# Kernel tuning notes

Measured on AMD Instinct MI355X. Metric: run time of the kernel, lower is better.

## Reference

```python
import jax, jax.numpy as jnp
import numpy as np

DIM = 512
HEAD_DIM = 32
HEADS = DIM // HEAD_DIM
WS = 7              # window_size
DISP = WS // 2      # cyclic shift displacement
SHIFTED = True


def _rel_indices(ws):
    # torch indexes pos_embedding with raw (possibly negative) distances;
    # negative python indices wrap modulo the dim size (2*ws-1).
    idx = np.array([[x, y] for x in range(ws) for y in range(ws)])
    d = idx[None, :, :] - idx[:, None, :]          # (ws^2, ws^2, 2)
    return np.mod(d, 2 * ws - 1)


def _mask(ws, disp, upper_lower, left_right):
    m = np.zeros((ws, ws, ws, ws), np.float32)
    if upper_lower:
        m[:-disp, :, -disp:, :] = -np.inf
        m[-disp:, :, :-disp, :] = -np.inf
    if left_right:
        m[:, -disp:, :, :-disp] = -np.inf
        m[:, :-disp, :, -disp:] = -np.inf
    return m.reshape(ws * ws, ws * ws)


def setup_inputs() -> dict:
    key = jax.random.key(0)
    ks = jax.random.split(key, 5)
    B, H, W = 32, 56, 56
    x = jax.random.normal(ks[0], (B, H, W, DIM), jnp.float32)
    w_qkv = jax.random.normal(ks[1], (DIM, 3 * DIM), jnp.float32) * 0.02
    pos_emb = jax.random.normal(ks[2], (2 * WS - 1, 2 * WS - 1, HEADS), jnp.float32)
    w_out = jax.random.normal(ks[3], (DIM, DIM), jnp.float32) * 0.02
    b_out = jax.random.normal(ks[4], (DIM,), jnp.float32) * 0.02
    return {"x": x, "w_qkv": w_qkv, "pos_emb": pos_emb, "w_out": w_out, "b_out": b_out}


def reference(x, w_qkv, pos_emb, w_out, b_out):
    rel = _rel_indices(WS)                         # static int constants
    ul_mask = jnp.asarray(_mask(WS, DISP, True, False))
    lr_mask = jnp.asarray(_mask(WS, DISP, False, True))

    B, H, W, _ = x.shape
    nw_h, nw_w = H // WS, W // WS

    if SHIFTED:
        x = jnp.roll(x, (-DISP, -DISP), axis=(1, 2))

    qkv = x @ w_qkv                                # (B,H,W,3*dim)

    def to_windows(t):
        # (B,H,W,dim) -> (B, heads, nw_h*nw_w, ws*ws, head_dim)
        t = t.reshape(B, nw_h, WS, nw_w, WS, HEADS, HEAD_DIM)
        return t.transpose(0, 5, 1, 3, 2, 4, 6).reshape(B, HEADS, nw_h * nw_w, WS * WS, HEAD_DIM)

    q, k, v = (to_windows(t) for t in jnp.split(qkv, 3, axis=-1))

    dots = jnp.einsum('bhwid,bhwjd->bhwij', q, k) * (HEAD_DIM ** -0.5)
    bias = pos_emb[rel[:, :, 0], rel[:, :, 1], :]  # (ws^2, ws^2, heads)
    dots = dots + bias.transpose(2, 0, 1)[None, :, None]

    if SHIFTED:
        dots = dots.at[:, :, -nw_w:].add(ul_mask)
        dots = dots.at[:, :, nw_w - 1::nw_w].add(lr_mask)

    attn = jax.nn.softmax(dots, axis=-1)
    out = jnp.einsum('bhwij,bhwjd->bhwid', attn, v)

    # (B,heads,nw,ws^2,d) -> (B,H,W,dim)
    out = out.reshape(B, HEADS, nw_h, nw_w, WS, WS, HEAD_DIM)
    out = out.transpose(0, 2, 4, 3, 5, 1, 6).reshape(B, H, W, DIM)
    out = out @ w_out + b_out

    if SHIFTED:
        out = jnp.roll(out, (DISP, DISP), axis=(1, 2))
    return out
```

## Files before the change

kernel.cpp:

```cpp
#include <hip/hip_runtime.h>
#include <hip/hip_bf16.h>
#include <stdint.h>


#define NWIN 64
#define NTOK 49
#define WIN_ELEMS 1568
#define HEAD_STRIDE 100352
#define BATCH_STRIDE 1605632
#define QKV_ELEMS 51380224
#define NTOKENS 100352
#define SCALE 0.17677669529663687f

typedef __attribute__((ext_vector_type(8))) short bf16x8;
typedef __attribute__((ext_vector_type(4))) float f32x4;

#define AS1 __attribute__((address_space(1)))
#define AS3 __attribute__((address_space(3)))

struct __align__(16) bf8 { __hip_bfloat16 h[8]; };

__device__ __forceinline__ void gload_lds16(const void* g, void* l) {
  __builtin_amdgcn_global_load_lds((const AS1 unsigned int*)g,
                                   (AS3 unsigned int*)l, 16, 0, 0);
}

__device__ __forceinline__ void token_decode(int t, int& b, int& i, int& j) {
  b = t / 3136;
  int r = t - b * 3136;
  i = r / 56;
  j = r - i * 56;
}

__global__ __launch_bounds__(256) void k_prep_lut(int* __restrict__ lutw,
                                                  int* __restrict__ luto) {
  int t = blockIdx.x * 256 + threadIdx.x;
  int b, i, j;
  token_decode(t, b, i, j);
  int win = (i / 7) * 8 + (j / 7);
  int pos = (i % 7) * 7 + (j % 7);
  lutw[t] = b * BATCH_STRIDE + win * WIN_ELEMS + pos * 32;
  int di = i + 3; if (di >= 56) di -= 56;
  int dj = j + 3; if (dj >= 56) dj -= 56;
  luto[t] = ((b * 56 + di) * 56 + dj) * 512;
}

__global__ __launch_bounds__(256) void k_prep_x(const float* __restrict__ x,
                                                __hip_bfloat16* __restrict__ xb) {
  int idx = blockIdx.x * 256 + threadIdx.x;
  int t = idx >> 6;
  int g = idx & 63;
  int b, i, j;
  token_decode(t, b, i, j);
  int si = i + 3; if (si >= 56) si -= 56;
  int sj = j + 3; if (sj >= 56) sj -= 56;
  const float* src = x + ((size_t)(b * 56 + si) * 56 + sj) * 512 + g * 8;
  float4 a0 = *(const float4*)src;
  float4 a1 = *(const float4*)(src + 4);
  bf8 o;
  o.h[0] = __float2bfloat16(a0.x); o.h[1] = __float2bfloat16(a0.y);
  o.h[2] = __float2bfloat16(a0.z); o.h[3] = __float2bfloat16(a0.w);
  o.h[4] = __float2bfloat16(a1.x); o.h[5] = __float2bfloat16(a1.y);
  o.h[6] = __float2bfloat16(a1.z); o.h[7] = __float2bfloat16(a1.w);
  int slot = ((g * 8) ^ ((t & 7) << 3));
  *(bf8*)(xb + (size_t)t * 512 + slot) = o;
}

__global__ __launch_bounds__(256) void k_transpose(const float* __restrict__ in,
                                                   __hip_bfloat16* __restrict__ out,
                                                   int K, int N) {
  __shared__ float tl[64][65];
  const int nb = blockIdx.x * 64, kb = blockIdx.y * 64;
  const int tid = threadIdx.x;
#pragma unroll
  for (int s = 0; s < 16; ++s) {
    int idx = s * 256 + tid; int r = idx >> 6, c = idx & 63;
    tl[r][c] = in[(size_t)(kb + r) * N + nb + c];
  }
  __syncthreads();
#pragma unroll
  for (int s = 0; s < 16; ++s) {
    int idx = s * 256 + tid; int r = idx >> 6, c = idx & 63;
    int row = nb + r;
    int col = (kb + c) ^ ((row & 7) << 3);
    out[(size_t)row * K + col] = __float2bfloat16(tl[c][r]);
  }
}

__global__ __launch_bounds__(256) void k_prep_bias(const float* __restrict__ pe,
                                                   float* __restrict__ biasT) {
  int id = blockIdx.x * 256 + threadIdx.x;
  int whid = id >> 12;
  int wtype = whid >> 4, h = whid & 15;
  int mid = id & 4095;
  int mf = mid >> 10, r = (mid >> 8) & 3, lane = (mid >> 2) & 63, nf = mid & 3;
  int key = mf * 16 + (lane >> 4) * 4 + r;
  int query = nf * 16 + (lane & 15);
  float v;
  if (key >= 49 || query >= 49) {
    v = -1e30f;
  } else {
    int i = query, j = key;
    int xi = i / 7, yi = i - xi * 7;
    int xj = j / 7, yj = j - xj * 7;
    int dx = xj - xi; if (dx < 0) dx += 13;
    int dy = yj - yi; if (dy < 0) dy += 13;
    v = pe[(dx * 13 + dy) * 16 + h];
    if ((wtype & 1) && ((xi >= 4) != (xj >= 4))) v = -1e30f;
    if ((wtype & 2) && ((yi >= 4) != (yj >= 4))) v = -1e30f;
  }
  biasT[id] = v;
}

__global__ __launch_bounds__(256) void k_qkv_mfma(
    const __hip_bfloat16* __restrict__ xb, const __hip_bfloat16* __restrict__ wbt,
    const int* __restrict__ lutw,
    __hip_bfloat16* __restrict__ qb, __hip_bfloat16* __restrict__ kb,
    __hip_bfloat16* __restrict__ vb) {
  __shared__ __align__(16) short As[2][128 * 64];
  __shared__ __align__(16) short Bs[2][128 * 64];
  const int tid = threadIdx.x;
  const int lid = blockIdx.x;
  const int wid = (lid & 7) * 1176 + (lid >> 3);
  const int t0 = (wid / 12) * 128;
  const int n0 = (wid % 12) * 128;
  const int lane = tid & 63, wave = tid >> 6;
  const int wm = wave >> 1, wn = wave & 1;

  const __hip_bfloat16* asrc[4];
  const __hip_bfloat16* bsrc[4];
#pragma unroll
  for (int s = 0; s < 4; ++s) {
    int c = s * 256 + tid;
    int row = c >> 3, kc = c & 7;
    asrc[s] = xb + (size_t)(t0 + row) * 512 + kc * 8;
    bsrc[s] = wbt + (size_t)(n0 + row) * 512 + kc * 8;
  }

  f32x4 acc[4][4] = {};
  const int arow = wm * 64 + (lane & 15);
  const int brow = wn * 64 + (lane & 15);
  const int koff = (lane >> 4) * 8;
  const int sw = (lane & 7) << 3;

#pragma unroll
  for (int s = 0; s < 4; ++s) {
    gload_lds16(asrc[s], (char*)As[0] + wave * 1024 + s * 4096);
    gload_lds16(bsrc[s], (char*)Bs[0] + wave * 1024 + s * 4096);
  }

  for (int t = 0; t < 8; ++t) {
    const int buf = t & 1;
    if (t < 7) {
      const int kt = (t + 1) * 64;
#pragma unroll
      for (int s = 0; s < 4; ++s) {
        gload_lds16(asrc[s] + kt, (char*)As[buf ^ 1] + wave * 1024 + s * 4096);
        gload_lds16(bsrc[s] + kt, (char*)Bs[buf ^ 1] + wave * 1024 + s * 4096);
      }
      asm volatile("s_waitcnt vmcnt(8)" ::: "memory");
    } else {
      asm volatile("s_waitcnt vmcnt(0)" ::: "memory");
    }
    __builtin_amdgcn_s_barrier();
    __builtin_amdgcn_sched_barrier(0);

    bf16x8 af[2][4], bfr[2][4];
#pragma unroll
    for (int kk = 0; kk < 2; ++kk) {
      const int eo = (kk * 32 + koff) ^ sw;
#pragma unroll
      for (int mf = 0; mf < 4; ++mf)
        af[kk][mf] = *(const bf16x8*)&As[buf][(arow + mf * 16) * 64 + eo];
#pragma unroll
      for (int nf = 0; nf < 4; ++nf)
        bfr[kk][nf] = *(const bf16x8*)&Bs[buf][(brow + nf * 16) * 64 + eo];
    }
    __builtin_amdgcn_s_setprio(1);
#pragma unroll
    for (int kk = 0; kk < 2; ++kk)
#pragma unroll
      for (int mf = 0; mf < 4; ++mf)
#pragma unroll
        for (int nf = 0; nf < 4; ++nf)
          acc[mf][nf] = __builtin_amdgcn_mfma_f32_16x16x32_bf16(
              af[kk][mf], bfr[kk][nf], acc[mf][nf], 0, 0, 0);
    __builtin_amdgcn_s_setprio(0);
    __builtin_amdgcn_s_barrier();
    __builtin_amdgcn_sched_barrier(0);
  }

  __hip_bfloat16* obs[4];
#pragma unroll
  for (int nf = 0; nf < 4; ++nf) {
    int n = n0 + wn * 64 + nf * 16 + (lane & 15);
    int sp = n >> 9, hc = n & 511, h = hc >> 5, d = hc & 31;
    obs[nf] = (sp == 0 ? qb : (sp == 1 ? kb : vb)) + (size_t)h * HEAD_STRIDE + d;
  }
  const int tbase = t0 + wm * 64 + (lane >> 4) * 4;
  int woff[4][4];
#pragma unroll
  for (int mf = 0; mf < 4; ++mf)
#pragma unroll
    for (int r = 0; r < 4; ++r)
      woff[mf][r] = lutw[tbase + mf * 16 + r];
#pragma unroll
  for (int mf = 0; mf < 4; ++mf)
#pragma unroll
    for (int r = 0; r < 4; ++r) {
      size_t off = (size_t)woff[mf][r];
#pragma unroll
      for (int nf = 0; nf < 4; ++nf)
        obs[nf][off] = __float2bfloat16(acc[mf][nf][r]);
    }
}

__global__ __launch_bounds__(256) void k_attn_mfma(
    const __hip_bfloat16* __restrict__ qb, const __hip_bfloat16* __restrict__ kb,
    const __hip_bfloat16* __restrict__ vb, const float* __restrict__ biasT,
    __hip_bfloat16* __restrict__ ab) {
  __shared__ __align__(16) __hip_bfloat16 P[4][64 * 72];
  __shared__ __align__(16) __hip_bfloat16 VT[4][32 * 64];
  const int tid = threadIdx.x, lane = tid & 63, wave = tid >> 6;
  const int gid = blockIdx.x * 4 + wave;
  const int win = gid & 63, h = (gid >> 6) & 15;
  const int wtype = (((win >> 3) == 7) ? 1 : 0) | (((win & 7) == 7) ? 2 : 0);
  const size_t qkbase = (size_t)gid * WIN_ELEMS;
  const int fr = lane & 15, fo = (lane >> 4) * 8;

  bf8 v8[4];
#pragma unroll
  for (int it = 0; it < 4; ++it) {
    int c = it * 64 + lane;
    if (c < 196) v8[it] = *(const bf8*)(vb + qkbase + (size_t)c * 8);
  }

  bf16x8 kf[4], qf[4];
#pragma unroll
  for (int f = 0; f < 4; ++f) {
    kf[f] = *(const bf16x8*)(kb + qkbase + (size_t)(f * 16 + fr) * 32 + fo);
    qf[f] = *(const bf16x8*)(qb + qkbase + (size_t)(f * 16 + fr) * 32 + fo);
  }

  __hip_bfloat16* vtw = VT[wave];
  {
    bf16x8 zz = {};
#pragma unroll
    for (int z = 0; z < 4; ++z) *(bf16x8*)&vtw[z * 512 + lane * 8] = zz;
  }
#pragma unroll
  for (int it = 0; it < 4; ++it) {
    int c = it * 64 + lane;
    if (c < 196) {
      int pos = c >> 2, d0 = (c & 3) * 8;
#pragma unroll
      for (int u = 0; u < 8; ++u) {
        int d = d0 + u;
        vtw[d * 64 + (pos ^ ((d & 7) << 3))] = v8[it].h[u];
      }
    }
  }

  f32x4 sacc[4][4] = {};
#pragma unroll
  for (int mf = 0; mf < 4; ++mf)
#pragma unroll
    for (int nf = 0; nf < 4; ++nf)
      sacc[mf][nf] = __builtin_amdgcn_mfma_f32_16x16x32_bf16(
          kf[mf], qf[nf], sacc[mf][nf], 0, 0, 0);

  const float* bp = biasT + (size_t)(wtype * 16 + h) * 4096;
#pragma unroll
  for (int mf = 0; mf < 4; ++mf)
#pragma unroll
    for (int r = 0; r < 4; ++r) {
      float4 bv = *(const float4*)(bp + ((mf * 4 + r) * 64 + lane) * 4);
      sacc[mf][0][r] = fmaf(sacc[mf][0][r], SCALE, bv.x);
      sacc[mf][1][r] = fmaf(sacc[mf][1][r], SCALE, bv.y);
      sacc[mf][2][r] = fmaf(sacc[mf][2][r], SCALE, bv.z);
      sacc[mf][3][r] = fmaf(sacc[mf][3][r], SCALE, bv.w);
    }

  float inv[4];
#pragma unroll
  for (int nf = 0; nf < 4; ++nf) {
    float m = sacc[0][nf][0];
#pragma unroll
    for (int mf = 0; mf < 4; ++mf)
#pragma unroll
      for (int r = 0; r < 4; ++r) m = fmaxf(m, sacc[mf][nf][r]);
    m = fmaxf(m, __shfl_xor(m, 16));
    m = fmaxf(m, __shfl_xor(m, 32));
    float sum = 0.f;
#pragma unroll
    for (int mf = 0; mf < 4; ++mf)
#pragma unroll
      for (int r = 0; r < 4; ++r) {
        float e = __expf(sacc[mf][nf][r] - m);
        sacc[mf][nf][r] = e;
        sum += e;
      }
    sum += __shfl_xor(sum, 16);
    sum += __shfl_xor(sum, 32);
    inv[nf] = 1.0f / sum;
  }

  __hip_bfloat16* pw = P[wave];
#pragma unroll
  for (int mf = 0; mf < 4; ++mf)
#pragma unroll
    for (int r = 0; r < 4; ++r) {
      int key = mf * 16 + (lane >> 4) * 4 + r;
#pragma unroll
      for (int nf = 0; nf < 4; ++nf) {
        int query = nf * 16 + fr;
        pw[query * 72 + key] = __float2bfloat16(sacc[mf][nf][r] * inv[nf]);
      }
    }

  f32x4 oacc[4][2] = {};
#pragma unroll
  for (int kk = 0; kk < 2; ++kk) {
    bf16x8 vf[2];
#pragma unroll
    for (int n2 = 0; n2 < 2; ++n2) {
      int d = n2 * 16 + fr;
      vf[n2] = *(const bf16x8*)&vtw[d * 64 + ((kk * 32 + fo) ^ ((d & 7) << 3))];
    }
#pragma unroll
    for (int mf = 0; mf < 4; ++mf) {
      bf16x8 pa = *(const bf16x8*)&pw[(mf * 16 + fr) * 72 + kk * 32 + fo];
#pragma unroll
      for (int n2 = 0; n2 < 2; ++n2)
        oacc[mf][n2] = __builtin_amdgcn_mfma_f32_16x16x32_bf16(
            pa, vf[n2], oacc[mf][n2], 0, 0, 0);
    }
  }

#pragma unroll
  for (int mf = 0; mf < 4; ++mf)
#pragma unroll
    for (int r = 0; r < 4; ++r) {
      int row = mf * 16 + (lane >> 4) * 4 + r;
      if (row < 49) {
#pragma unroll
        for (int n2 = 0; n2 < 2; ++n2)
          ab[qkbase + (size_t)row * 32 + n2 * 16 + fr] =
              __float2bfloat16(oacc[mf][n2][r]);
      }
    }
}

__global__ __launch_bounds__(256) void k_out_mfma(
    const __hip_bfloat16* __restrict__ ab, const __hip_bfloat16* __restrict__ wot,
    const int* __restrict__ lutw, const int* __restrict__ luto,
    const float* __restrict__ bias, float* __restrict__ out) {
  __shared__ __align__(16) short As[2][128 * 64];
  __shared__ __align__(16) short Bs[2][128 * 64];
  const int tid = threadIdx.x;
  const int lid = blockIdx.x;
  const int wid = (lid & 7) * 392 + (lid >> 3);
  const int t0 = (wid >> 2) * 128;
  const int n0 = (wid & 3) * 128;
  const int lane = tid & 63, wave = tid >> 6;
  const int wm = wave >> 1, wn = wave & 1;

  size_t aoff[4];
  const __hip_bfloat16* bsrc[4];
#pragma unroll
  for (int s = 0; s < 4; ++s) {
    int c = s * 256 + tid;
    int row = c >> 3, kc = c & 7;
    aoff[s] = (size_t)lutw[t0 + row] + (size_t)(kc >> 2) * HEAD_STRIDE + (kc & 3) * 8;
    bsrc[s] = wot + (size_t)(n0 + row) * 512 + kc * 8;
  }

  f32x4 acc[4][4] = {};
  const int arow = wm * 64 + (lane & 15);
  const int brow = wn * 64 + (lane & 15);
  const int koff = (lane >> 4) * 8;
  const int sw = (lane & 7) << 3;

#pragma unroll
  for (int s = 0; s < 4; ++s) {
    gload_lds16(ab + aoff[s], (char*)As[0] + wave * 1024 + s * 4096);
    gload_lds16(bsrc[s], (char*)Bs[0] + wave * 1024 + s * 4096);
  }

  for (int t = 0; t < 8; ++t) {
    const int buf = t & 1;
    if (t < 7) {
      const int kt = (t + 1) * 64;
      size_t hoff = (size_t)(kt >> 5) * HEAD_STRIDE;
#pragma unroll
      for (int s = 0; s < 4; ++s) {
        gload_lds16(ab + aoff[s] + hoff, (char*)As[buf ^ 1] + wave * 1024 + s * 4096);
        gload_lds16(bsrc[s] + kt, (char*)Bs[buf ^ 1] + wave * 1024 + s * 4096);
      }
      asm volatile("s_waitcnt vmcnt(8)" ::: "memory");
    } else {
      asm volatile("s_waitcnt vmcnt(0)" ::: "memory");
    }
    __builtin_amdgcn_s_barrier();
    __builtin_amdgcn_sched_barrier(0);

    bf16x8 af[2][4], bfr[2][4];
#pragma unroll
    for (int kk = 0; kk < 2; ++kk) {
      const int eo = kk * 32 + koff;
#pragma unroll
      for (int mf = 0; mf < 4; ++mf)
        af[kk][mf] = *(const bf16x8*)&As[buf][(arow + mf * 16) * 64 + eo];
#pragma unroll
      for (int nf = 0; nf < 4; ++nf)
        bfr[kk][nf] = *(const bf16x8*)&Bs[buf][(brow + nf * 16) * 64 + (eo ^ sw)];
    }
    __builtin_amdgcn_s_setprio(1);
#pragma unroll
    for (int kk = 0; kk < 2; ++kk)
#pragma unroll
      for (int mf = 0; mf < 4; ++mf)
#pragma unroll
        for (int nf = 0; nf < 4; ++nf)
          acc[mf][nf] = __builtin_amdgcn_mfma_f32_16x16x32_bf16(
              af[kk][mf], bfr[kk][nf], acc[mf][nf], 0, 0, 0);
    __builtin_amdgcn_s_setprio(0);
    __builtin_amdgcn_s_barrier();
    __builtin_amdgcn_sched_barrier(0);
  }

  float bia[4];
#pragma unroll
  for (int nf = 0; nf < 4; ++nf)
    bia[nf] = bias[n0 + wn * 64 + nf * 16 + (lane & 15)];

  const int tbase = t0 + wm * 64 + (lane >> 4) * 4;
  int ooff[4][4];
#pragma unroll
  for (int mf = 0; mf < 4; ++mf)
#pragma unroll
    for (int r = 0; r < 4; ++r)
      ooff[mf][r] = luto[tbase + mf * 16 + r];
#pragma unroll
  for (int mf = 0; mf < 4; ++mf) {
#pragma unroll
    for (int r = 0; r < 4; ++r) {
      float* op = out + (size_t)ooff[mf][r] + n0 + wn * 64 + (lane & 15);
#pragma unroll
      for (int nf = 0; nf < 4; ++nf) op[nf * 16] = acc[mf][nf][r] + bia[nf];
    }
  }
}

extern "C" void kernel_launch(void* const* d_in, const int* in_sizes, int n_in,
                              void* d_out, int out_size, void* d_ws, size_t ws_size,
                              hipStream_t stream) {
  const float* x     = (const float*)d_in[0];
  const float* w_qkv = (const float*)d_in[1];
  const float* pe    = (const float*)d_in[2];
  const float* w_out = (const float*)d_in[3];
  const float* b_out = (const float*)d_in[4];
  float* out = (float*)d_out;

  __hip_bfloat16* qb  = (__hip_bfloat16*)d_ws;
  __hip_bfloat16* kb  = qb + (size_t)QKV_ELEMS;
  __hip_bfloat16* vb  = kb + (size_t)QKV_ELEMS;
  __hip_bfloat16* xb  = vb + (size_t)QKV_ELEMS;
  __hip_bfloat16* ab  = xb;
  __hip_bfloat16* wbt = xb + (size_t)QKV_ELEMS;
  __hip_bfloat16* wot = wbt + (size_t)(1536 * 512);
  float* biasT = (float*)(wot + (size_t)(512 * 512));
  int* lutw = (int*)(biasT + 262144);
  int* luto = lutw + NTOKENS;

  k_prep_lut<<<dim3(392), dim3(256), 0, stream>>>(lutw, luto);
  k_prep_x<<<dim3(25088), dim3(256), 0, stream>>>(x, xb);
  k_transpose<<<dim3(24, 8), dim3(256), 0, stream>>>(w_qkv, wbt, 512, 1536);
  k_transpose<<<dim3(8, 8), dim3(256), 0, stream>>>(w_out, wot, 512, 512);
  k_prep_bias<<<dim3(1024), dim3(256), 0, stream>>>(pe, biasT);
  k_qkv_mfma<<<dim3(9408), dim3(256), 0, stream>>>(xb, wbt, lutw, qb, kb, vb);
  k_attn_mfma<<<dim3(8192), dim3(256), 0, stream>>>(qb, kb, vb, biasT, ab);
  k_out_mfma<<<dim3(3136), dim3(256), 0, stream>>>(ab, wot, lutw, luto, b_out, out);
}
```

Baseline: 542.4 us.

## Fuse shifted fp32-to-bf16 input conversion into QKV GEMM A-tile loading

```diff
diff --git a/kernel.cpp b/kernel.cpp
--- a/kernel.cpp
+++ b/kernel.cpp
@@ -32,38 +32,28 @@
   j = r - i * 56;
 }
 
-__global__ __launch_bounds__(256) void k_prep_lut(int* __restrict__ lutw,
+__device__ __forceinline__ bf8 pack8(const float4& a, const float4& b) {
+  bf8 o;
+  o.h[0] = __float2bfloat16(a.x); o.h[1] = __float2bfloat16(a.y);
+  o.h[2] = __float2bfloat16(a.z); o.h[3] = __float2bfloat16(a.w);
+  o.h[4] = __float2bfloat16(b.x); o.h[5] = __float2bfloat16(b.y);
+  o.h[6] = __float2bfloat16(b.z); o.h[7] = __float2bfloat16(b.w);
+  return o;
+}
+
+__global__ __launch_bounds__(256) void k_prep_lut(int* __restrict__ lutr,
+                                                  int* __restrict__ lutw,
                                                   int* __restrict__ luto) {
   int t = blockIdx.x * 256 + threadIdx.x;
   int b, i, j;
   token_decode(t, b, i, j);
+  int si = i + 3; if (si >= 56) si -= 56;
+  int sj = j + 3; if (sj >= 56) sj -= 56;
+  lutr[t] = ((b * 56 + si) * 56 + sj) * 512;
   int win = (i / 7) * 8 + (j / 7);
   int pos = (i % 7) * 7 + (j % 7);
   lutw[t] = b * BATCH_STRIDE + win * WIN_ELEMS + pos * 32;
-  int di = i + 3; if (di >= 56) di -= 56;
-  int dj = j + 3; if (dj >= 56) dj -= 56;
-  luto[t] = ((b * 56 + di) * 56 + dj) * 512;
-}
-
-__global__ __launch_bounds__(256) void k_prep_x(const float* __restrict__ x,
-                                                __hip_bfloat16* __restrict__ xb) {
-  int idx = blockIdx.x * 256 + threadIdx.x;
-  int t = idx >> 6;
-  int g = idx & 63;
-  int b, i, j;
-  token_decode(t, b, i, j);
-  int si = i + 3; if (si >= 56) si -= 56;
-  int sj = j + 3; if (sj >= 56) sj -= 56;
-  const float* src = x + ((size_t)(b * 56 + si) * 56 + sj) * 512 + g * 8;
-  float4 a0 = *(const float4*)src;
-  float4 a1 = *(const float4*)(src + 4);
-  bf8 o;
-  o.h[0] = __float2bfloat16(a0.x); o.h[1] = __float2bfloat16(a0.y);
-  o.h[2] = __float2bfloat16(a0.z); o.h[3] = __float2bfloat16(a0.w);
-  o.h[4] = __float2bfloat16(a1.x); o.h[5] = __float2bfloat16(a1.y);
-  o.h[6] = __float2bfloat16(a1.z); o.h[7] = __float2bfloat16(a1.w);
-  int slot = ((g * 8) ^ ((t & 7) << 3));
-  *(bf8*)(xb + (size_t)t * 512 + slot) = o;
+  luto[t] = lutr[t];
 }
 
 __global__ __launch_bounds__(256) void k_transpose(const float* __restrict__ in,
@@ -113,8 +103,8 @@
 }
 
 __global__ __launch_bounds__(256) void k_qkv_mfma(
-    const __hip_bfloat16* __restrict__ xb, const __hip_bfloat16* __restrict__ wbt,
-    const int* __restrict__ lutw,
+    const float* __restrict__ x, const __hip_bfloat16* __restrict__ wbt,
+    const int* __restrict__ lutr, const int* __restrict__ lutw,
     __hip_bfloat16* __restrict__ qb, __hip_bfloat16* __restrict__ kb,
     __hip_bfloat16* __restrict__ vb) {
   __shared__ __align__(16) short As[2][128 * 64];
@@ -127,13 +117,19 @@
   const int lane = tid & 63, wave = tid >> 6;
   const int wm = wave >> 1, wn = wave & 1;
 
-  const __hip_bfloat16* asrc[4];
+  const int arow_s = tid >> 1, half = tid & 1;
+  const float* axp = x + (size_t)lutr[t0 + arow_s] + half * 32;
+  short* aw[2] = { &As[0][arow_s * 64], &As[1][arow_s * 64] };
+  int wch[4];
+#pragma unroll
+  for (int c = 0; c < 4; ++c)
+    wch[c] = ((half * 4 + c) ^ (arow_s & 7)) * 8;
+
   const __hip_bfloat16* bsrc[4];
 #pragma unroll
   for (int s = 0; s < 4; ++s) {
     int c = s * 256 + tid;
     int row = c >> 3, kc = c & 7;
-    asrc[s] = xb + (size_t)(t0 + row) * 512 + kc * 8;
     bsrc[s] = wbt + (size_t)(n0 + row) * 512 + kc * 8;
   }
 
@@ -143,22 +139,28 @@
   const int koff = (lane >> 4) * 8;
   const int sw = (lane & 7) << 3;
 
-#pragma unroll
-  for (int s = 0; s < 4; ++s) {
-    gload_lds16(asrc[s], (char*)As[0] + wave * 1024 + s * 4096);
+  float4 ar[8];
+#pragma unroll
+  for (int u = 0; u < 8; ++u) ar[u] = ((const float4*)axp)[u];
+#pragma unroll
+  for (int s = 0; s < 4; ++s)
     gload_lds16(bsrc[s], (char*)Bs[0] + wave * 1024 + s * 4096);
-  }
+#pragma unroll
+  for (int c = 0; c < 4; ++c)
+    *(bf8*)(aw[0] + wch[c]) = pack8(ar[2 * c], ar[2 * c + 1]);
+  asm volatile("s_waitcnt lgkmcnt(0)" ::: "memory");
 
   for (int t = 0; t < 8; ++t) {
     const int buf = t & 1;
     if (t < 7) {
       const int kt = (t + 1) * 64;
-#pragma unroll
-      for (int s = 0; s < 4; ++s) {
-        gload_lds16(asrc[s] + kt, (char*)As[buf ^ 1] + wave * 1024 + s * 4096);
+      const float* p = axp + kt;
+#pragma unroll
+      for (int u = 0; u < 8; ++u) ar[u] = ((const float4*)p)[u];
+#pragma unroll
+      for (int s = 0; s < 4; ++s)
         gload_lds16(bsrc[s] + kt, (char*)Bs[buf ^ 1] + wave * 1024 + s * 4096);
-      }
-      asm volatile("s_waitcnt vmcnt(8)" ::: "memory");
+      asm volatile("s_waitcnt vmcnt(12)" ::: "memory");
     } else {
       asm volatile("s_waitcnt vmcnt(0)" ::: "memory");
     }
@@ -186,6 +188,12 @@
           acc[mf][nf] = __builtin_amdgcn_mfma_f32_16x16x32_bf16(
               af[kk][mf], bfr[kk][nf], acc[mf][nf], 0, 0, 0);
     __builtin_amdgcn_s_setprio(0);
+    if (t < 7) {
+#pragma unroll
+      for (int c = 0; c < 4; ++c)
+        *(bf8*)(aw[buf ^ 1] + wch[c]) = pack8(ar[2 * c], ar[2 * c + 1]);
+    }
+    asm volatile("s_waitcnt lgkmcnt(0)" ::: "memory");
     __builtin_amdgcn_s_barrier();
     __builtin_amdgcn_sched_barrier(0);
   }
@@ -465,20 +473,19 @@
   __hip_bfloat16* qb  = (__hip_bfloat16*)d_ws;
   __hip_bfloat16* kb  = qb + (size_t)QKV_ELEMS;
   __hip_bfloat16* vb  = kb + (size_t)QKV_ELEMS;
-  __hip_bfloat16* xb  = vb + (size_t)QKV_ELEMS;
-  __hip_bfloat16* ab  = xb;
-  __hip_bfloat16* wbt = xb + (size_t)QKV_ELEMS;
+  __hip_bfloat16* ab  = vb + (size_t)QKV_ELEMS;
+  __hip_bfloat16* wbt = ab + (size_t)QKV_ELEMS;
   __hip_bfloat16* wot = wbt + (size_t)(1536 * 512);
   float* biasT = (float*)(wot + (size_t)(512 * 512));
-  int* lutw = (int*)(biasT + 262144);
+  int* lutr = (int*)(biasT + 262144);
+  int* lutw = lutr + NTOKENS;
   int* luto = lutw + NTOKENS;
 
-  k_prep_lut<<<dim3(392), dim3(256), 0, stream>>>(lutw, luto);
-  k_prep_x<<<dim3(25088), dim3(256), 0, stream>>>(x, xb);
+  k_prep_lut<<<dim3(392), dim3(256), 0, stream>>>(lutr, lutw, luto);
   k_transpose<<<dim3(24, 8), dim3(256), 0, stream>>>(w_qkv, wbt, 512, 1536);
   k_transpose<<<dim3(8, 8), dim3(256), 0, stream>>>(w_out, wot, 512, 512);
   k_prep_bias<<<dim3(1024), dim3(256), 0, stream>>>(pe, biasT);
-  k_qkv_mfma<<<dim3(9408), dim3(256), 0, stream>>>(xb, wbt, lutw, qb, kb, vb);
+  k_qkv_mfma<<<dim3(9408), dim3(256), 0, stream>>>(x, wbt, lutr, lutw, qb, kb, vb);
   k_attn_mfma<<<dim3(8192), dim3(256), 0, stream>>>(qb, kb, vb, biasT, ab);
   k_out_mfma<<<dim3(3136), dim3(256), 0, stream>>>(ab, wot, lutw, luto, b_out, out);
 }
```

Result: slower. 870.3 us (+60.5%).

## Enlarge QKV GEMM tile to 256x128, drop double buffering, coarsen x prep

Applied to the files above, without the earlier changes.

```diff
diff --git a/kernel.cpp b/kernel.cpp
--- a/kernel.cpp
+++ b/kernel.cpp
@@ -48,22 +48,27 @@
 __global__ __launch_bounds__(256) void k_prep_x(const float* __restrict__ x,
                                                 __hip_bfloat16* __restrict__ xb) {
   int idx = blockIdx.x * 256 + threadIdx.x;
-  int t = idx >> 6;
-  int g = idx & 63;
+  int t = idx >> 4;
+  int q = idx & 15;
   int b, i, j;
   token_decode(t, b, i, j);
   int si = i + 3; if (si >= 56) si -= 56;
   int sj = j + 3; if (sj >= 56) sj -= 56;
-  const float* src = x + ((size_t)(b * 56 + si) * 56 + sj) * 512 + g * 8;
-  float4 a0 = *(const float4*)src;
-  float4 a1 = *(const float4*)(src + 4);
-  bf8 o;
-  o.h[0] = __float2bfloat16(a0.x); o.h[1] = __float2bfloat16(a0.y);
-  o.h[2] = __float2bfloat16(a0.z); o.h[3] = __float2bfloat16(a0.w);
-  o.h[4] = __float2bfloat16(a1.x); o.h[5] = __float2bfloat16(a1.y);
-  o.h[6] = __float2bfloat16(a1.z); o.h[7] = __float2bfloat16(a1.w);
-  int slot = ((g * 8) ^ ((t & 7) << 3));
-  *(bf8*)(xb + (size_t)t * 512 + slot) = o;
+  const float* src = x + ((size_t)(b * 56 + si) * 56 + sj) * 512 + q * 32;
+  __hip_bfloat16* dst = xb + (size_t)t * 512;
+  const int rsw = t & 7;
+#pragma unroll
+  for (int c = 0; c < 4; ++c) {
+    float4 a0 = *(const float4*)(src + c * 8);
+    float4 a1 = *(const float4*)(src + c * 8 + 4);
+    bf8 o;
+    o.h[0] = __float2bfloat16(a0.x); o.h[1] = __float2bfloat16(a0.y);
+    o.h[2] = __float2bfloat16(a0.z); o.h[3] = __float2bfloat16(a0.w);
+    o.h[4] = __float2bfloat16(a1.x); o.h[5] = __float2bfloat16(a1.y);
+    o.h[6] = __float2bfloat16(a1.z); o.h[7] = __float2bfloat16(a1.w);
+    int g = q * 4 + c;
+    *(bf8*)(dst + ((g ^ rsw) << 3)) = o;
+  }
 }
 
 __global__ __launch_bounds__(256) void k_transpose(const float* __restrict__ in,
@@ -117,77 +122,63 @@
     const int* __restrict__ lutw,
     __hip_bfloat16* __restrict__ qb, __hip_bfloat16* __restrict__ kb,
     __hip_bfloat16* __restrict__ vb) {
-  __shared__ __align__(16) short As[2][128 * 64];
-  __shared__ __align__(16) short Bs[2][128 * 64];
+  __shared__ __align__(16) short As[256 * 64];
+  __shared__ __align__(16) short Bs[128 * 64];
   const int tid = threadIdx.x;
   const int lid = blockIdx.x;
-  const int wid = (lid & 7) * 1176 + (lid >> 3);
-  const int t0 = (wid / 12) * 128;
+  const int wid = (lid & 7) * 588 + (lid >> 3);
+  const int t0 = (wid / 12) * 256;
   const int n0 = (wid % 12) * 128;
   const int lane = tid & 63, wave = tid >> 6;
   const int wm = wave >> 1, wn = wave & 1;
 
-  const __hip_bfloat16* asrc[4];
+  const __hip_bfloat16* asrc[8];
+#pragma unroll
+  for (int s = 0; s < 8; ++s) {
+    int c = s * 256 + tid;
+    int row = c >> 3, kc = c & 7;
+    asrc[s] = xb + (size_t)(t0 + row) * 512 + kc * 8;
+  }
   const __hip_bfloat16* bsrc[4];
 #pragma unroll
   for (int s = 0; s < 4; ++s) {
     int c = s * 256 + tid;
     int row = c >> 3, kc = c & 7;
-    asrc[s] = xb + (size_t)(t0 + row) * 512 + kc * 8;
     bsrc[s] = wbt + (size_t)(n0 + row) * 512 + kc * 8;
   }
 
-  f32x4 acc[4][4] = {};
-  const int arow = wm * 64 + (lane & 15);
+  f32x4 acc[8][4] = {};
+  const int arow = wm * 128 + (lane & 15);
   const int brow = wn * 64 + (lane & 15);
   const int koff = (lane >> 4) * 8;
   const int sw = (lane & 7) << 3;
 
-#pragma unroll
-  for (int s = 0; s < 4; ++s) {
-    gload_lds16(asrc[s], (char*)As[0] + wave * 1024 + s * 4096);
-    gload_lds16(bsrc[s], (char*)Bs[0] + wave * 1024 + s * 4096);
-  }
-
-  for (int t = 0; t < 8; ++t) {
-    const int buf = t & 1;
-    if (t < 7) {
-      const int kt = (t + 1) * 64;
-#pragma unroll
-      for (int s = 0; s < 4; ++s) {
-        gload_lds16(asrc[s] + kt, (char*)As[buf ^ 1] + wave * 1024 + s * 4096);
-        gload_lds16(bsrc[s] + kt, (char*)Bs[buf ^ 1] + wave * 1024 + s * 4096);
-      }
-      asm volatile("s_waitcnt vmcnt(8)" ::: "memory");
-    } else {
-      asm volatile("s_waitcnt vmcnt(0)" ::: "memory");
-    }
-    __builtin_amdgcn_s_barrier();
-    __builtin_amdgcn_sched_barrier(0);
-
-    bf16x8 af[2][4], bfr[2][4];
+  for (int kt = 0; kt < 512; kt += 64) {
+#pragma unroll
+    for (int s = 0; s < 8; ++s)
+      gload_lds16(asrc[s] + kt, (char*)As + s * 4096 + wave * 1024);
+#pragma unroll
+    for (int s = 0; s < 4; ++s)
+      gload_lds16(bsrc[s] + kt, (char*)Bs + s * 4096 + wave * 1024);
+    __syncthreads();
 #pragma unroll
     for (int kk = 0; kk < 2; ++kk) {
       const int eo = (kk * 32 + koff) ^ sw;
-#pragma unroll
-      for (int mf = 0; mf < 4; ++mf)
-        af[kk][mf] = *(const bf16x8*)&As[buf][(arow + mf * 16) * 64 + eo];
+      bf16x8 af[8], bfr[4];
 #pragma unroll
       for (int nf = 0; nf < 4; ++nf)
-        bfr[kk][nf] = *(const bf16x8*)&Bs[buf][(brow + nf * 16) * 64 + eo];
-    }
-    __builtin_amdgcn_s_setprio(1);
-#pragma unroll
-    for (int kk = 0; kk < 2; ++kk)
-#pragma unroll
-      for (int mf = 0; mf < 4; ++mf)
+        bfr[nf] = *(const bf16x8*)&Bs[(brow + nf * 16) * 64 + eo];
+#pragma unroll
+      for (int mf = 0; mf < 8; ++mf)
+        af[mf] = *(const bf16x8*)&As[(arow + mf * 16) * 64 + eo];
+#pragma unroll
+      for (int mf = 0; mf < 8; ++mf)
 #pragma unroll
         for (int nf = 0; nf < 4; ++nf)
           acc[mf][nf] = __builtin_amdgcn_mfma_f32_16x16x32_bf16(
-              af[kk][mf], bfr[kk][nf], acc[mf][nf], 0, 0, 0);
-    __builtin_amdgcn_s_setprio(0);
-    __builtin_amdgcn_s_barrier();
-    __builtin_amdgcn_sched_barrier(0);
+              af[mf], bfr[nf], acc[mf][nf], 0, 0, 0);
+    }
+    __syncthreads();
   }
 
   __hip_bfloat16* obs[4];
@@ -197,22 +188,17 @@
     int sp = n >> 9, hc = n & 511, h = hc >> 5, d = hc & 31;
     obs[nf] = (sp == 0 ? qb : (sp == 1 ? kb : vb)) + (size_t)h * HEAD_STRIDE + d;
   }
-  const int tbase = t0 + wm * 64 + (lane >> 4) * 4;
-  int woff[4][4];
-#pragma unroll
-  for (int mf = 0; mf < 4; ++mf)
-#pragma unroll
-    for (int r = 0; r < 4; ++r)
-      woff[mf][r] = lutw[tbase + mf * 16 + r];
-#pragma unroll
-  for (int mf = 0; mf < 4; ++mf)
+  const int tbase = t0 + wm * 128 + (lane >> 4) * 4;
+#pragma unroll
+  for (int mf = 0; mf < 8; ++mf) {
 #pragma unroll
     for (int r = 0; r < 4; ++r) {
-      size_t off = (size_t)woff[mf][r];
+      size_t off = (size_t)lutw[tbase + mf * 16 + r];
 #pragma unroll
       for (int nf = 0; nf < 4; ++nf)
         obs[nf][off] = __float2bfloat16(acc[mf][nf][r]);
     }
+  }
 }
 
 __global__ __launch_bounds__(256) void k_attn_mfma(
@@ -474,11 +460,11 @@
   int* luto = lutw + NTOKENS;
 
   k_prep_lut<<<dim3(392), dim3(256), 0, stream>>>(lutw, luto);
-  k_prep_x<<<dim3(25088), dim3(256), 0, stream>>>(x, xb);
+  k_prep_x<<<dim3(6272), dim3(256), 0, stream>>>(x, xb);
   k_transpose<<<dim3(24, 8), dim3(256), 0, stream>>>(w_qkv, wbt, 512, 1536);
   k_transpose<<<dim3(8, 8), dim3(256), 0, stream>>>(w_out, wot, 512, 512);
   k_prep_bias<<<dim3(1024), dim3(256), 0, stream>>>(pe, biasT);
-  k_qkv_mfma<<<dim3(9408), dim3(256), 0, stream>>>(xb, wbt, lutw, qb, kb, vb);
+  k_qkv_mfma<<<dim3(4704), dim3(256), 0, stream>>>(xb, wbt, lutw, qb, kb, vb);
   k_attn_mfma<<<dim3(8192), dim3(256), 0, stream>>>(qb, kb, vb, biasT, ab);
   k_out_mfma<<<dim3(3136), dim3(256), 0, stream>>>(ab, wot, lutw, luto, b_out, out);
 }
```

New measurement: 629.2 us. 16.0% more time.

## Enlarge QKV GEMM tile to 256x128 with triple-buffered interleaved prefetch

Applied to the files above, without the earlier changes.

```diff
diff --git a/kernel.cpp b/kernel.cpp
--- a/kernel.cpp
+++ b/kernel.cpp
@@ -112,30 +112,34 @@
   biasT[id] = v;
 }
 
-__global__ __launch_bounds__(256) void k_qkv_mfma(
+__global__ __launch_bounds__(512) void k_qkv_mfma(
     const __hip_bfloat16* __restrict__ xb, const __hip_bfloat16* __restrict__ wbt,
     const int* __restrict__ lutw,
     __hip_bfloat16* __restrict__ qb, __hip_bfloat16* __restrict__ kb,
     __hip_bfloat16* __restrict__ vb) {
-  __shared__ __align__(16) short As[2][128 * 64];
-  __shared__ __align__(16) short Bs[2][128 * 64];
+  __shared__ __align__(16) short As[3][256 * 64];
+  __shared__ __align__(16) short Bs[3][128 * 64];
   const int tid = threadIdx.x;
   const int lid = blockIdx.x;
-  const int wid = (lid & 7) * 1176 + (lid >> 3);
-  const int t0 = (wid / 12) * 128;
+  const int wid = (lid & 7) * 588 + (lid >> 3);
+  const int t0 = (wid / 12) * 256;
   const int n0 = (wid % 12) * 128;
   const int lane = tid & 63, wave = tid >> 6;
   const int wm = wave >> 1, wn = wave & 1;
 
   const __hip_bfloat16* asrc[4];
-  const __hip_bfloat16* bsrc[4];
 #pragma unroll
   for (int s = 0; s < 4; ++s) {
-    int c = s * 256 + tid;
-    int row = c >> 3, kc = c & 7;
-    asrc[s] = xb + (size_t)(t0 + row) * 512 + kc * 8;
-    bsrc[s] = wbt + (size_t)(n0 + row) * 512 + kc * 8;
-  }
+    int c = s * 512 + tid;
+    asrc[s] = xb + (size_t)(t0 + (c >> 3)) * 512 + (c & 7) * 8;
+  }
+  const __hip_bfloat16* bsrc[2];
+#pragma unroll
+  for (int s = 0; s < 2; ++s) {
+    int c = s * 512 + tid;
+    bsrc[s] = wbt + (size_t)(n0 + (c >> 3)) * 512 + (c & 7) * 8;
+  }
+  const int lofs = wave * 1024;
 
   f32x4 acc[4][4] = {};
   const int arow = wm * 64 + (lane & 15);
@@ -144,50 +148,77 @@
   const int sw = (lane & 7) << 3;
 
 #pragma unroll
-  for (int s = 0; s < 4; ++s) {
-    gload_lds16(asrc[s], (char*)As[0] + wave * 1024 + s * 4096);
-    gload_lds16(bsrc[s], (char*)Bs[0] + wave * 1024 + s * 4096);
-  }
-
+  for (int s = 0; s < 4; ++s) gload_lds16(asrc[s], (char*)As[0] + s * 8192 + lofs);
+#pragma unroll
+  for (int s = 0; s < 2; ++s) gload_lds16(bsrc[s], (char*)Bs[0] + s * 8192 + lofs);
+#pragma unroll
+  for (int s = 0; s < 4; ++s) gload_lds16(asrc[s] + 64, (char*)As[1] + s * 8192 + lofs);
+#pragma unroll
+  for (int s = 0; s < 2; ++s) gload_lds16(bsrc[s] + 64, (char*)Bs[1] + s * 8192 + lofs);
+
+  int bufc = 0;
   for (int t = 0; t < 8; ++t) {
-    const int buf = t & 1;
-    if (t < 7) {
-      const int kt = (t + 1) * 64;
-#pragma unroll
-      for (int s = 0; s < 4; ++s) {
-        gload_lds16(asrc[s] + kt, (char*)As[buf ^ 1] + wave * 1024 + s * 4096);
-        gload_lds16(bsrc[s] + kt, (char*)Bs[buf ^ 1] + wave * 1024 + s * 4096);
-      }
-      asm volatile("s_waitcnt vmcnt(8)" ::: "memory");
-    } else {
-      asm volatile("s_waitcnt vmcnt(0)" ::: "memory");
-    }
+    if (t == 7) asm volatile("s_waitcnt vmcnt(0)" ::: "memory");
+    else        asm volatile("s_waitcnt vmcnt(6)" ::: "memory");
     __builtin_amdgcn_s_barrier();
     __builtin_amdgcn_sched_barrier(0);
-
-    bf16x8 af[2][4], bfr[2][4];
-#pragma unroll
-    for (int kk = 0; kk < 2; ++kk) {
-      const int eo = (kk * 32 + koff) ^ sw;
+    const short* Ab = As[bufc];
+    const short* Bb = Bs[bufc];
+    const int bufs = (bufc + 2 >= 3) ? bufc - 1 : bufc + 2;
+    const int kts = (t + 2) * 64;
+    const bool pf = (t < 6);
+
+    {
+      const int eo = koff ^ sw;
+      bf16x8 af[4], bfr[4];
 #pragma unroll
       for (int mf = 0; mf < 4; ++mf)
-        af[kk][mf] = *(const bf16x8*)&As[buf][(arow + mf * 16) * 64 + eo];
+        af[mf] = *(const bf16x8*)&Ab[(arow + mf * 16) * 64 + eo];
 #pragma unroll
       for (int nf = 0; nf < 4; ++nf)
-        bfr[kk][nf] = *(const bf16x8*)&Bs[buf][(brow + nf * 16) * 64 + eo];
-    }
-    __builtin_amdgcn_s_setprio(1);
-#pragma unroll
-    for (int kk = 0; kk < 2; ++kk)
+        bfr[nf] = *(const bf16x8*)&Bb[(brow + nf * 16) * 64 + eo];
+      if (pf) {
+        gload_lds16(asrc[0] + kts, (char*)As[bufs] + 0 * 8192 + lofs);
+        gload_lds16(asrc[1] + kts, (char*)As[bufs] + 1 * 8192 + lofs);
+        gload_lds16(asrc[2] + kts, (char*)As[bufs] + 2 * 8192 + lofs);
+      }
+      asm volatile("s_waitcnt lgkmcnt(0)" ::: "memory");
+      __builtin_amdgcn_sched_barrier(0);
+      __builtin_amdgcn_s_setprio(1);
 #pragma unroll
       for (int mf = 0; mf < 4; ++mf)
 #pragma unroll
         for (int nf = 0; nf < 4; ++nf)
           acc[mf][nf] = __builtin_amdgcn_mfma_f32_16x16x32_bf16(
-              af[kk][mf], bfr[kk][nf], acc[mf][nf], 0, 0, 0);
-    __builtin_amdgcn_s_setprio(0);
-    __builtin_amdgcn_s_barrier();
-    __builtin_amdgcn_sched_barrier(0);
+              af[mf], bfr[nf], acc[mf][nf], 0, 0, 0);
+      __builtin_amdgcn_s_setprio(0);
+    }
+    {
+      const int eo = (32 + koff) ^ sw;
+      bf16x8 af[4], bfr[4];
+#pragma unroll
+      for (int mf = 0; mf < 4; ++mf)
+        af[mf] = *(const bf16x8*)&Ab[(arow + mf * 16) * 64 + eo];
+#pragma unroll
+      for (int nf = 0; nf < 4; ++nf)
+        bfr[nf] = *(const bf16x8*)&Bb[(brow + nf * 16) * 64 + eo];
+      if (pf) {
+        gload_lds16(asrc[3] + kts, (char*)As[bufs] + 3 * 8192 + lofs);
+        gload_lds16(bsrc[0] + kts, (char*)Bs[bufs] + 0 * 8192 + lofs);
+        gload_lds16(bsrc[1] + kts, (char*)Bs[bufs] + 1 * 8192 + lofs);
+      }
+      asm volatile("s_waitcnt lgkmcnt(0)" ::: "memory");
+      __builtin_amdgcn_sched_barrier(0);
+      __builtin_amdgcn_s_setprio(1);
+#pragma unroll
+      for (int mf = 0; mf < 4; ++mf)
+#pragma unroll
+        for (int nf = 0; nf < 4; ++nf)
+          acc[mf][nf] = __builtin_amdgcn_mfma_f32_16x16x32_bf16(
+              af[mf], bfr[nf], acc[mf][nf], 0, 0, 0);
+      __builtin_amdgcn_s_setprio(0);
+    }
+    bufc = (bufc == 2) ? 0 : bufc + 1;
   }
 
   __hip_bfloat16* obs[4];
@@ -262,12 +293,14 @@
   }
 
   f32x4 sacc[4][4] = {};
+  __builtin_amdgcn_s_setprio(1);
 #pragma unroll
   for (int mf = 0; mf < 4; ++mf)
 #pragma unroll
     for (int nf = 0; nf < 4; ++nf)
       sacc[mf][nf] = __builtin_amdgcn_mfma_f32_16x16x32_bf16(
           kf[mf], qf[nf], sacc[mf][nf], 0, 0, 0);
+  __builtin_amdgcn_s_setprio(0);
 
   const float* bp = biasT + (size_t)(wtype * 16 + h) * 4096;
 #pragma unroll
@@ -327,6 +360,7 @@
       int d = n2 * 16 + fr;
       vf[n2] = *(const bf16x8*)&vtw[d * 64 + ((kk * 32 + fo) ^ ((d & 7) << 3))];
     }
+    __builtin_amdgcn_s_setprio(1);
 #pragma unroll
     for (int mf = 0; mf < 4; ++mf) {
       bf16x8 pa = *(const bf16x8*)&pw[(mf * 16 + fr) * 72 + kk * 32 + fo];
@@ -335,6 +369,7 @@
         oacc[mf][n2] = __builtin_amdgcn_mfma_f32_16x16x32_bf16(
             pa, vf[n2], oacc[mf][n2], 0, 0, 0);
     }
+    __builtin_amdgcn_s_setprio(0);
   }
 
 #pragma unroll
@@ -478,7 +513,7 @@
   k_transpose<<<dim3(24, 8), dim3(256), 0, stream>>>(w_qkv, wbt, 512, 1536);
   k_transpose<<<dim3(8, 8), dim3(256), 0, stream>>>(w_out, wot, 512, 512);
   k_prep_bias<<<dim3(1024), dim3(256), 0, stream>>>(pe, biasT);
-  k_qkv_mfma<<<dim3(9408), dim3(256), 0, stream>>>(xb, wbt, lutw, qb, kb, vb);
+  k_qkv_mfma<<<dim3(4704), dim3(512), 0, stream>>>(xb, wbt, lutw, qb, kb, vb);
   k_attn_mfma<<<dim3(8192), dim3(256), 0, stream>>>(qb, kb, vb, biasT, ab);
   k_out_mfma<<<dim3(3136), dim3(256), 0, stream>>>(ab, wot, lutw, luto, b_out, out);
 }
```

Result: no change. 550.9 us (+1.6%).
